# Performance work log

Measured on AMD Instinct MI355X. Metric: run time of the kernel, lower is better.

The kernel has to match this reference:

```python
import jax, jax.numpy as jnp
import numpy as np

HEADS = 8
DIM_HEAD = 64
SCALE = DIM_HEAD ** -0.5
K = 7


def _conv(x, w, stride):
    return jax.lax.conv_general_dilated(
        x, w, window_strides=(stride, stride), padding='VALID',
        dimension_numbers=('NHWC', 'HWIO', 'NHWC'))


def _split_heads(t):
    # 'b x y (h d) -> (b h) (x y) d'
    b, X, Y, hd = t.shape
    d = hd // HEADS
    t = t.reshape(b, X, Y, HEADS, d)
    t = t.transpose(0, 3, 1, 2, 4)  # b h x y d
    return t.reshape(b * HEADS, X * Y, d)


def setup_inputs() -> dict:
    key = jax.random.key(0)
    ks = jax.random.split(key, 6)
    dim, inner = 256, HEADS * DIM_HEAD
    x = jax.random.normal(ks[0], (8, 84, 84, dim), dtype=jnp.float32)
    w_q = jax.random.normal(ks[1], (1, 1, dim, inner), dtype=jnp.float32) * 0.02
    w_kv = jax.random.normal(ks[2], (K, K, dim, 2 * inner), dtype=jnp.float32) * 0.02
    w_out = jax.random.normal(ks[3], (1, 1, inner, dim), dtype=jnp.float32) * 0.02
    b_out = jnp.zeros((dim,), dtype=jnp.float32)
    return {"x": x, "w_q": w_q, "w_kv": w_kv, "w_out": w_out, "b_out": b_out}


def reference(x, w_q, w_kv, w_out, b_out):
    b, X, Y, _ = x.shape
    q = _conv(x, w_q, 1)          # [b, X, Y, inner]
    kv = _conv(x, w_kv, K)        # [b, X/k, Y/k, 2*inner]
    k, v = jnp.split(kv, 2, axis=-1)
    q = _split_heads(q)           # [(b h), XY, d]
    k = _split_heads(k)           # [(b h), xy, d]
    v = _split_heads(v)
    dots = jnp.einsum('bid,bjd->bij', q, k) * SCALE
    attn = jax.nn.softmax(dots, axis=-1)
    out = jnp.einsum('bij,bjd->bid', attn, v)  # [(b h), XY, d]
    out = out.reshape(b, HEADS, X, Y, DIM_HEAD).transpose(0, 2, 3, 1, 4)
    out = out.reshape(b, X, Y, HEADS * DIM_HEAD)
    out = _conv(out, w_out, 1) + b_out  # dropout rate 0 -> identity
    return out
```

## Files before the change

### kernel.cpp

```cpp
#include <hip/hip_runtime.h>

typedef unsigned short u16;
typedef __bf16 bf16x8 __attribute__((ext_vector_type(8)));
typedef __bf16 bf16x4 __attribute__((ext_vector_type(4)));
typedef float f32x4 __attribute__((ext_vector_type(4)));

__device__ __forceinline__ u16 f2b(float f) {
    __bf16 h = (__bf16)f;
    return __builtin_bit_cast(u16, h);
}
__device__ __forceinline__ unsigned pk2(float a, float b) {
    return (unsigned)f2b(a) | ((unsigned)f2b(b) << 16);
}

__device__ __forceinline__ int xcd_chunk(int wg, int n) {
    int q = n >> 3, r = n & 7;
    int x = wg & 7, i = wg >> 3;
    return (x < r ? x * (q + 1) : r * (q + 1) + (x - r) * q) + i;
}

#define GLOAD_LDS16(src, dst)                                              \
    __builtin_amdgcn_global_load_lds(                                      \
        (const __attribute__((address_space(1))) void*)(src),              \
        (__attribute__((address_space(3))) void*)(dst), 16, 0, 0)

__global__ __launch_bounds__(256) void k_pack_x(const float* __restrict__ x,
                                                u16* __restrict__ xp) {
    int v = blockIdx.x * 256 + threadIdx.x;
    int c0 = (v & 31) << 3;
    int pix = v >> 5;
    int b = pix / 7056;
    int r = pix - b * 7056;
    int y = r / 84;
    int xx = r - y * 84;
    int opix = (b * 144 + (y / 7) * 12 + (xx / 7)) * 49 + (y % 7) * 7 + (xx % 7);
    const float4* src = reinterpret_cast<const float4*>(x + ((size_t)pix << 8) + c0);
    float4 f0 = src[0], f1 = src[1];
    bf16x8 o = {(__bf16)f0.x, (__bf16)f0.y, (__bf16)f0.z, (__bf16)f0.w,
                (__bf16)f1.x, (__bf16)f1.y, (__bf16)f1.z, (__bf16)f1.w};
    *reinterpret_cast<bf16x8*>(xp + ((size_t)opix << 8) + c0) = o;
}

__global__ __launch_bounds__(256) void k_lut(int* __restrict__ lut) {
    int q = blockIdx.x * 256 + threadIdx.x;
    if (q >= 7056) return;
    int pi = q / 49, pos = q - pi * 49;
    int y = (pi / 12) * 7 + pos / 7;
    int xx = (pi - (pi / 12) * 12) * 7 + (pos - (pos / 7) * 7);
    lut[q] = y * 84 + xx;
}

__global__ __launch_bounds__(256) void k_tconv(const float* __restrict__ in,
                                               u16* __restrict__ out, int R, int C,
                                               float scale, int permk) {
    __shared__ float tile[32][33];
    int c0 = blockIdx.x << 5, r0 = blockIdx.y << 5;
    int tx = threadIdx.x, ty = threadIdx.y;
#pragma unroll
    for (int i = 0; i < 4; i++)
        tile[ty + (i << 3)][tx] = in[(size_t)(r0 + ty + (i << 3)) * C + c0 + tx];
    __syncthreads();
    int k = r0 + tx;
    int kw = permk ? ((k & ~63) | ((k & 15) << 2) | ((k >> 4) & 3)) : k;
#pragma unroll
    for (int i = 0; i < 4; i++)
        out[(size_t)(c0 + ty + (i << 3)) * R + kw] = f2b(tile[tx][ty + (i << 3)] * scale);
}

__global__ __launch_bounds__(256) void k_kvproj(const u16* __restrict__ xp,
                                                const u16* __restrict__ wkvT,
                                                float* __restrict__ parts) {
    __shared__ u16 As[8192];
    __shared__ u16 Bs[8192];
    const int lin = xcd_chunk(blockIdx.x, 504);
    const int mt = lin % 9;
    const int rest = lin / 9;
    const int nt = rest & 7;
    const int sp = rest >> 3;
    const int tid = threadIdx.x;
    const int wave = tid >> 6, lane = tid & 63;
    const int wr = wave >> 1, wc = wave & 1;
    const int lrow = lane & 15, lkg = lane >> 4;
    const u16* Ag = xp + (size_t)(mt * 128) * 12544 + sp * 1792;
    const u16* Bg = wkvT + (size_t)(nt * 128) * 12544 + sp * 1792;
    const int srow = lane >> 3;
    const int scol_sw = (((lane & 7) ^ srow) << 3);
    f32x4 acc[4][4];
#pragma unroll
    for (int m = 0; m < 4; m++)
#pragma unroll
        for (int n = 0; n < 4; n++)
#pragma unroll
            for (int i = 0; i < 4; i++) acc[m][n][i] = 0.f;

    for (int ks = 0; ks < 28; ks++) {
        const int k0 = ks << 6;
        __syncthreads();
#pragma unroll
        for (int j = 0; j < 4; j++) {
            const int c = (wave << 2) + j;
            const int row = (c << 3) + srow;
            GLOAD_LDS16(Ag + (size_t)row * 12544 + k0 + scol_sw, As + (c << 9));
            GLOAD_LDS16(Bg + (size_t)row * 12544 + k0 + scol_sw, Bs + (c << 9));
        }
        __syncthreads();
#pragma unroll
        for (int kk = 0; kk < 2; kk++) {
            const int sig = (kk << 2) + lkg;
            const int sw = ((sig ^ (lrow & 7)) << 3);
            bf16x8 a[4], bb[4];
#pragma unroll
            for (int m = 0; m < 4; m++)
                a[m] = *reinterpret_cast<const bf16x8*>(As + (((wr << 6) + (m << 4) + lrow) << 6) + sw);
#pragma unroll
            for (int n = 0; n < 4; n++)
                bb[n] = *reinterpret_cast<const bf16x8*>(Bs + (((wc << 6) + (n << 4) + lrow) << 6) + sw);
#pragma unroll
            for (int m = 0; m < 4; m++)
#pragma unroll
                for (int n = 0; n < 4; n++)
                    acc[m][n] = __builtin_amdgcn_mfma_f32_16x16x32_bf16(a[m], bb[n], acc[m][n], 0, 0, 0);
        }
    }
    float* outp = parts + (size_t)sp * 1179648;
#pragma unroll
    for (int m = 0; m < 4; m++)
#pragma unroll
        for (int n = 0; n < 4; n++)
#pragma unroll
            for (int i = 0; i < 4; i++) {
                int row = (mt << 7) + (wr << 6) + (m << 4) + (lkg << 2) + i;
                int col = (nt << 7) + (wc << 6) + (n << 4) + lrow;
                outp[(size_t)row * 1024 + col] = acc[m][n][i];
            }
}

__global__ __launch_bounds__(256) void k_kvfin(const float* __restrict__ parts,
                                               u16* __restrict__ Kf, u16* __restrict__ Vf) {
    int v = blockIdx.x * 256 + threadIdx.x;
    int m = v >> 8;
    int n0 = (v & 255) << 2;
    float4 s = {0.f, 0.f, 0.f, 0.f};
#pragma unroll
    for (int sp = 0; sp < 7; sp++) {
        float4 p = *reinterpret_cast<const float4*>(parts + (size_t)sp * 1179648 +
                                                    (size_t)m * 1024 + n0);
        s.x += p.x; s.y += p.y; s.z += p.z; s.w += p.w;
    }
    int b = m / 144, pi = m - b * 144;
    float sv[4] = {s.x, s.y, s.z, s.w};
#pragma unroll
    for (int e4 = 0; e4 < 4; e4++) {
        int n = n0 + e4;
        int h = (n & 511) >> 6, d = n & 63;
        int bh = (b << 3) + h;
        if (n < 512) {
            int fc = pi >> 4, lr = pi & 15;
            int ks = d >> 5, lg = (d >> 3) & 3, e = d & 7;
            Kf[((((size_t)bh * 9 + fc) << 1) + ks) * 512 + (((lg << 4) + lr) << 3) + e] = f2b(sv[e4]);
        } else {
            int nf = d >> 4, lr = d & 15;
            int ks = pi >> 5;
            int e = (((pi >> 4) & 1) << 2) | (pi & 3);
            int lg = (pi >> 2) & 3;
            Vf[(((size_t)bh * 4 + nf) * 5 + ks) * 512 + (((lg << 4) + lr) << 3) + e] = f2b(sv[e4]);
        }
    }
}

__global__ __launch_bounds__(256) void k_qproj(const u16* __restrict__ xp,
                                               const u16* __restrict__ wqT,
                                               u16* __restrict__ Qf) {
    __shared__ u16 As[8192];
    __shared__ u16 Bs[8192];
    const int lin = xcd_chunk(blockIdx.x, 1764);
    const int nt = lin & 3, mt = lin >> 2;
    const int tid = threadIdx.x;
    const int wave = tid >> 6, lane = tid & 63;
    const int wr = wave >> 1, wc = wave & 1;
    const int lrow = lane & 15, lkg = lane >> 4;
    const u16* Ag = xp + (size_t)(mt * 128) * 256;
    const u16* Bg = wqT + (size_t)(nt * 128) * 256;
    const int srow = lane >> 3;
    const int scol_sw = (((lane & 7) ^ srow) << 3);
    f32x4 acc[4][4];
#pragma unroll
    for (int m = 0; m < 4; m++)
#pragma unroll
        for (int n = 0; n < 4; n++)
#pragma unroll
            for (int i = 0; i < 4; i++) acc[m][n][i] = 0.f;

    for (int ks = 0; ks < 4; ks++) {
        const int k0 = ks << 6;
        __syncthreads();
#pragma unroll
        for (int j = 0; j < 4; j++) {
            const int c = (wave << 2) + j;
            const int row = (c << 3) + srow;
            GLOAD_LDS16(Ag + (size_t)row * 256 + k0 + scol_sw, As + (c << 9));
            GLOAD_LDS16(Bg + (size_t)row * 256 + k0 + scol_sw, Bs + (c << 9));
        }
        __syncthreads();
#pragma unroll
        for (int kk = 0; kk < 2; kk++) {
            const int sig = (kk << 2) + lkg;
            const int sw = ((sig ^ (lrow & 7)) << 3);
            bf16x8 a[4], bb[4];
#pragma unroll
            for (int m = 0; m < 4; m++)
                a[m] = *reinterpret_cast<const bf16x8*>(As + (((wr << 6) + (m << 4) + lrow) << 6) + sw);
#pragma unroll
            for (int n = 0; n < 4; n++)
                bb[n] = *reinterpret_cast<const bf16x8*>(Bs + (((wc << 6) + (n << 4) + lrow) << 6) + sw);
#pragma unroll
            for (int m = 0; m < 4; m++)
#pragma unroll
                for (int n = 0; n < 4; n++)
                    acc[m][n] = __builtin_amdgcn_mfma_f32_16x16x32_bf16(a[m], bb[n], acc[m][n], 0, 0, 0);
        }
    }
#pragma unroll
    for (int m = 0; m < 4; m++)
#pragma unroll
        for (int n = 0; n < 4; n++)
#pragma unroll
            for (int i = 0; i < 4; i++) {
                int row = (mt << 7) + (wr << 6) + (m << 4) + (lkg << 2) + i;
                int col = (nt << 7) + (wc << 6) + (n << 4) + lrow;
                int b = row / 7056, pp = row - b * 7056;
                int h = col >> 6, d = col & 63;
                int bh = (b << 3) + h;
                int tt = pp >> 4, flr = pp & 15;
                int fks = d >> 5, flg = (d >> 3) & 3, fe = d & 7;
                Qf[((((size_t)bh * 441 + tt) << 1) + fks) * 512 + (((flg << 4) + flr) << 3) + fe] =
                    f2b(acc[m][n][i]);
            }
}

__global__ __launch_bounds__(128, 2) void k_attn(const u16* __restrict__ Qf,
                                                 const u16* __restrict__ Kf,
                                                 const u16* __restrict__ Vf,
                                                 const int* __restrict__ lut,
                                                 u16* __restrict__ O) {
    const int wv = threadIdx.x >> 6, lane = threadIdx.x & 63;
    const int h = (blockIdx.y << 1) + wv;
    const int b = blockIdx.z;
    const int lrow = lane & 15, lkg = lane >> 4;
    const int bh = (b << 3) + h;
    const int l8 = lane << 3;

    const u16* Kg = Kf + (((size_t)bh * 9) << 10);
    const u16* Vg = Vf + ((size_t)bh * 20) * 512;

    bf16x8 kf[9][2], vf[4][5];
#pragma unroll
    for (int fc = 0; fc < 9; fc++)
#pragma unroll
        for (int ks = 0; ks < 2; ks++)
            kf[fc][ks] = *reinterpret_cast<const bf16x8*>(Kg + (((fc << 1) + ks) << 9) + l8);
#pragma unroll
    for (int n = 0; n < 4; n++)
#pragma unroll
        for (int ks = 0; ks < 5; ks++)
            vf[n][ks] = *reinterpret_cast<const bf16x8*>(Vg + ((size_t)(n * 5 + ks) << 9) + l8);

    const int t0 = blockIdx.x * 3;
#pragma unroll 1
    for (int jt = 0; jt < 3; jt++) {
        const int t = t0 + jt;
        const u16* Qg = Qf + ((((size_t)bh * 441 + t) << 1) << 9);

        f32x4 da[9];
#pragma unroll
        for (int fc = 0; fc < 9; fc++)
#pragma unroll
            for (int i = 0; i < 4; i++) da[fc][i] = 0.f;
#pragma unroll
        for (int ks = 0; ks < 2; ks++) {
            bf16x8 aq = *reinterpret_cast<const bf16x8*>(Qg + (ks << 9) + l8);
#pragma unroll
            for (int fc = 0; fc < 9; fc++)
                da[fc] = __builtin_amdgcn_mfma_f32_16x16x32_bf16(kf[fc][ks], aq, da[fc], 0, 0, 0);
        }

        float mx = -1e30f;
#pragma unroll
        for (int fc = 0; fc < 9; fc++)
#pragma unroll
            for (int i = 0; i < 4; i++) mx = fmaxf(mx, da[fc][i]);
        mx = fmaxf(mx, __shfl_xor(mx, 16));
        mx = fmaxf(mx, __shfl_xor(mx, 32));
        float sum = 0.f;
#pragma unroll
        for (int fc = 0; fc < 9; fc++)
#pragma unroll
            for (int i = 0; i < 4; i++) {
                float v = __expf(da[fc][i] - mx);
                da[fc][i] = v;
                sum += v;
            }
        sum += __shfl_xor(sum, 16);
        sum += __shfl_xor(sum, 32);
        float inv = 1.0f / sum;
        unsigned pw[9][2];
#pragma unroll
        for (int fc = 0; fc < 9; fc++) {
            pw[fc][0] = pk2(da[fc][0] * inv, da[fc][1] * inv);
            pw[fc][1] = pk2(da[fc][2] * inv, da[fc][3] * inv);
        }

        f32x4 oa[4];
#pragma unroll
        for (int n = 0; n < 4; n++)
#pragma unroll
            for (int i = 0; i < 4; i++) oa[n][i] = 0.f;
#pragma unroll
        for (int ks = 0; ks < 5; ks++) {
            uint4 pav;
            if (ks < 4)
                pav = uint4{pw[2 * ks][0], pw[2 * ks][1], pw[2 * ks + 1][0], pw[2 * ks + 1][1]};
            else
                pav = uint4{pw[8][0], pw[8][1], 0u, 0u};
            bf16x8 pa = __builtin_bit_cast(bf16x8, pav);
#pragma unroll
            for (int n = 0; n < 4; n++)
                oa[n] = __builtin_amdgcn_mfma_f32_16x16x32_bf16(pa, vf[n][ks], oa[n], 0, 0, 0);
        }

#pragma unroll
        for (int i = 0; i < 4; i++) {
            int q = (t << 4) + (lkg << 2) + i;
            int rast = lut[q];
            bf16x4 ov = {(__bf16)oa[0][i], (__bf16)oa[1][i], (__bf16)oa[2][i], (__bf16)oa[3][i]};
            *reinterpret_cast<bf16x4*>(O + (((size_t)b * 7056 + rast) << 9) +
                                       (h << 6) + (lrow << 2)) = ov;
        }
    }
}

__global__ __launch_bounds__(256) void k_outproj(const u16* __restrict__ A,
                                                 const u16* __restrict__ BT,
                                                 const float* __restrict__ bias,
                                                 float* __restrict__ out) {
    __shared__ u16 As[128][72];
    __shared__ u16 Bs[128][72];
    const int lin = xcd_chunk(blockIdx.x, 882);
    const int nt = lin & 1, mt = lin >> 1;
    const int tid = threadIdx.x;
    const int wave = tid >> 6, lane = tid & 63;
    const int wr = wave >> 1, wc = wave & 1;
    const int lrow = lane & 15, lkg = lane >> 4;
    const u16* Ag = A + (size_t)(mt * 128) * 512;
    const u16* Bg = BT + (size_t)(nt * 128) * 512;
    const int srow = tid >> 3, scol = (tid & 7) << 3;
    f32x4 acc[4][4];
#pragma unroll
    for (int m = 0; m < 4; m++)
#pragma unroll
        for (int n = 0; n < 4; n++)
#pragma unroll
            for (int i = 0; i < 4; i++) acc[m][n][i] = 0.f;

    for (int ks = 0; ks < 8; ks++) {
        const int k0 = ks * 64;
        __syncthreads();
#pragma unroll
        for (int p = 0; p < 4; p++) {
            int rr = srow + (p << 5);
            *reinterpret_cast<bf16x8*>(&As[rr][scol]) =
                *reinterpret_cast<const bf16x8*>(Ag + (size_t)rr * 512 + k0 + scol);
            *reinterpret_cast<bf16x8*>(&Bs[rr][scol]) =
                *reinterpret_cast<const bf16x8*>(Bg + (size_t)rr * 512 + k0 + scol);
        }
        __syncthreads();
#pragma unroll
        for (int kk = 0; kk < 2; kk++) {
            const int ko = (kk << 5) + (lkg << 3);
            bf16x8 a[4], bb[4];
#pragma unroll
            for (int m = 0; m < 4; m++)
                a[m] = *reinterpret_cast<const bf16x8*>(&As[(wr << 6) + (m << 4) + lrow][ko]);
#pragma unroll
            for (int n = 0; n < 4; n++)
                bb[n] = *reinterpret_cast<const bf16x8*>(&Bs[(wc << 6) + (n << 4) + lrow][ko]);
#pragma unroll
            for (int m = 0; m < 4; m++)
#pragma unroll
                for (int n = 0; n < 4; n++)
                    acc[m][n] = __builtin_amdgcn_mfma_f32_16x16x32_bf16(a[m], bb[n], acc[m][n], 0, 0, 0);
        }
    }
#pragma unroll
    for (int m = 0; m < 4; m++)
#pragma unroll
        for (int n = 0; n < 4; n++)
#pragma unroll
            for (int i = 0; i < 4; i++) {
                int row = (mt << 7) + (wr << 6) + (m << 4) + (lkg << 2) + i;
                int col = (nt << 7) + (wc << 6) + (n << 4) + lrow;
                out[(size_t)row * 256 + col] = acc[m][n][i] + bias[col];
            }
}

extern "C" void kernel_launch(void* const* d_in, const int* in_sizes, int n_in,
                              void* d_out, int out_size, void* d_ws, size_t ws_size,
                              hipStream_t stream) {
    const float* x = (const float*)d_in[0];
    const float* w_q = (const float*)d_in[1];
    const float* w_kv = (const float*)d_in[2];
    const float* w_out = (const float*)d_in[3];
    const float* b_out = (const float*)d_in[4];
    float* out = (float*)d_out;

    char* ws = (char*)d_ws;
    size_t off = 0;
    auto alloc = [&](size_t bytes) -> char* {
        char* p = ws + off;
        off = (off + bytes + 255) & ~(size_t)255;
        return p;
    };
    u16* xp = (u16*)alloc(28901376ull);
    u16* wqT = (u16*)alloc(262144ull);
    u16* woutT = (u16*)alloc(262144ull);
    u16* Kf = (u16*)alloc(1179648ull);
    u16* Vf = (u16*)alloc(1310720ull);
    int* lut = (int*)alloc(28416ull);
    u16* O = (u16*)alloc(57802752ull);
    u16* wkvT = (u16*)alloc(25690112ull);
    float* parts = (float*)alloc(33030144ull);
    u16* Qf = (u16*)wkvT;

    hipMemsetAsync(Vf, 0, 1310720ull, stream);
    k_lut<<<28, 256, 0, stream>>>(lut);
    k_pack_x<<<7056, 256, 0, stream>>>(x, xp);
    k_tconv<<<dim3(32, 392), dim3(32, 8), 0, stream>>>(w_kv, wkvT, 12544, 1024, 1.0f, 0);
    k_tconv<<<dim3(16, 8), dim3(32, 8), 0, stream>>>(w_q, wqT, 256, 512, 0.125f, 0);
    k_tconv<<<dim3(8, 16), dim3(32, 8), 0, stream>>>(w_out, woutT, 512, 256, 1.0f, 1);
    k_kvproj<<<504, 256, 0, stream>>>(xp, wkvT, parts);
    k_kvfin<<<1152, 256, 0, stream>>>(parts, Kf, Vf);
    k_qproj<<<1764, 256, 0, stream>>>(xp, wqT, Qf);
    k_attn<<<dim3(147, 4, 8), 128, 0, stream>>>(Qf, Kf, Vf, lut, O);
    k_outproj<<<882, 256, 0, stream>>>(O, woutT, b_out, out);
}
```

Baseline: 205.0 us.

## Fuse output projection into attention kernel via shared-memory staging

Each attention block now runs all 8 heads for one batch and tile, writes the per-head outputs into shared memory, then multiplies them by a pre-fragmented w_out with MFMA and writes the final fp32 result plus bias directly. This removes the separate out-projection GEMM and the round trip of the large bf16 O intermediate through global memory. In exchange each block does extra synchronisation and reads w_out fragments from global or L2 on every tile. The block also grows to 512 threads, which may lower occupancy.

```diff
diff --git a/kernel.cpp b/kernel.cpp
--- a/kernel.cpp
+++ b/kernel.cpp
@@ -52,7 +52,7 @@
 
 __global__ __launch_bounds__(256) void k_tconv(const float* __restrict__ in,
                                                u16* __restrict__ out, int R, int C,
-                                               float scale, int permk) {
+                                               float scale) {
     __shared__ float tile[32][33];
     int c0 = blockIdx.x << 5, r0 = blockIdx.y << 5;
     int tx = threadIdx.x, ty = threadIdx.y;
@@ -61,10 +61,19 @@
         tile[ty + (i << 3)][tx] = in[(size_t)(r0 + ty + (i << 3)) * C + c0 + tx];
     __syncthreads();
     int k = r0 + tx;
-    int kw = permk ? ((k & ~63) | ((k & 15) << 2) | ((k >> 4) & 3)) : k;
 #pragma unroll
     for (int i = 0; i < 4; i++)
-        out[(size_t)(c0 + ty + (i << 3)) * R + kw] = f2b(tile[tx][ty + (i << 3)] * scale);
+        out[(size_t)(c0 + ty + (i << 3)) * R + k] = f2b(tile[tx][ty + (i << 3)] * scale);
+}
+
+__global__ __launch_bounds__(256) void k_wofrag(const float* __restrict__ w_out,
+                                               u16* __restrict__ woFrag) {
+    int v = blockIdx.x * 256 + threadIdx.x;
+    int k = v >> 8, outcol = v & 255;
+    int kw = (k & ~63) | ((k & 15) << 2) | ((k >> 4) & 3);
+    int nf = outcol >> 4, lr = outcol & 15;
+    int ks = kw >> 5, lg = (kw >> 3) & 3, e = kw & 7;
+    woFrag[((((nf << 4) + ks) << 6) + (lg << 4) + lr) * 8 + e] = f2b(w_out[v]);
 }
 
 __global__ __launch_bounds__(256) void k_kvproj(const u16* __restrict__ xp,
@@ -238,14 +247,17 @@
             }
 }
 
-__global__ __launch_bounds__(128, 2) void k_attn(const u16* __restrict__ Qf,
-                                                 const u16* __restrict__ Kf,
-                                                 const u16* __restrict__ Vf,
-                                                 const int* __restrict__ lut,
-                                                 u16* __restrict__ O) {
+__global__ __launch_bounds__(512, 2) void k_attn_out(const u16* __restrict__ Qf,
+                                                     const u16* __restrict__ Kf,
+                                                     const u16* __restrict__ Vf,
+                                                     const int* __restrict__ lut,
+                                                     const u16* __restrict__ woFrag,
+                                                     const float* __restrict__ bias,
+                                                     float* __restrict__ out) {
+    __shared__ u16 Osm[16 * 520];
     const int wv = threadIdx.x >> 6, lane = threadIdx.x & 63;
-    const int h = (blockIdx.y << 1) + wv;
-    const int b = blockIdx.z;
+    const int h = wv;
+    const int b = blockIdx.y;
     const int lrow = lane & 15, lkg = lane >> 4;
     const int bh = (b << 3) + h;
     const int l8 = lane << 3;
@@ -264,6 +276,10 @@
 #pragma unroll
         for (int ks = 0; ks < 5; ks++)
             vf[n][ks] = *reinterpret_cast<const bf16x8*>(Vg + ((size_t)(n * 5 + ks) << 9) + l8);
+
+    const int nf0 = wv << 1;
+    const float bias0 = bias[(nf0 << 4) + lrow];
+    const float bias1 = bias[((nf0 + 1) << 4) + lrow];
 
     const int t0 = blockIdx.x * 3;
 #pragma unroll 1
@@ -330,77 +346,32 @@
 
 #pragma unroll
         for (int i = 0; i < 4; i++) {
+            int q = (lkg << 2) + i;
+            bf16x4 ov = {(__bf16)oa[0][i], (__bf16)oa[1][i], (__bf16)oa[2][i], (__bf16)oa[3][i]};
+            *reinterpret_cast<bf16x4*>(&Osm[q * 520 + (h << 6) + (lrow << 2)]) = ov;
+        }
+        __syncthreads();
+
+        f32x4 oc0, oc1;
+#pragma unroll
+        for (int i = 0; i < 4; i++) { oc0[i] = 0.f; oc1[i] = 0.f; }
+#pragma unroll
+        for (int ks = 0; ks < 16; ks++) {
+            bf16x8 a = *reinterpret_cast<const bf16x8*>(&Osm[lrow * 520 + (ks << 5) + (lkg << 3)]);
+            bf16x8 b0 = *reinterpret_cast<const bf16x8*>(woFrag + ((((nf0 << 4) + ks) << 6) << 3) + l8);
+            bf16x8 b1 = *reinterpret_cast<const bf16x8*>(woFrag + (((((nf0 + 1) << 4) + ks) << 6) << 3) + l8);
+            oc0 = __builtin_amdgcn_mfma_f32_16x16x32_bf16(a, b0, oc0, 0, 0, 0);
+            oc1 = __builtin_amdgcn_mfma_f32_16x16x32_bf16(a, b1, oc1, 0, 0, 0);
+        }
+#pragma unroll
+        for (int i = 0; i < 4; i++) {
             int q = (t << 4) + (lkg << 2) + i;
-            int rast = lut[q];
-            bf16x4 ov = {(__bf16)oa[0][i], (__bf16)oa[1][i], (__bf16)oa[2][i], (__bf16)oa[3][i]};
-            *reinterpret_cast<bf16x4*>(O + (((size_t)b * 7056 + rast) << 9) +
-                                       (h << 6) + (lrow << 2)) = ov;
-        }
+            float* op = out + ((size_t)b * 7056 + lut[q]) * 256;
+            op[(nf0 << 4) + lrow] = oc0[i] + bias0;
+            op[((nf0 + 1) << 4) + lrow] = oc1[i] + bias1;
+        }
+        __syncthreads();
     }
-}
-
-__global__ __launch_bounds__(256) void k_outproj(const u16* __restrict__ A,
-                                                 const u16* __restrict__ BT,
-                                                 const float* __restrict__ bias,
-                                                 float* __restrict__ out) {
-    __shared__ u16 As[128][72];
-    __shared__ u16 Bs[128][72];
-    const int lin = xcd_chunk(blockIdx.x, 882);
-    const int nt = lin & 1, mt = lin >> 1;
-    const int tid = threadIdx.x;
-    const int wave = tid >> 6, lane = tid & 63;
-    const int wr = wave >> 1, wc = wave & 1;
-    const int lrow = lane & 15, lkg = lane >> 4;
-    const u16* Ag = A + (size_t)(mt * 128) * 512;
-    const u16* Bg = BT + (size_t)(nt * 128) * 512;
-    const int srow = tid >> 3, scol = (tid & 7) << 3;
-    f32x4 acc[4][4];
-#pragma unroll
-    for (int m = 0; m < 4; m++)
-#pragma unroll
-        for (int n = 0; n < 4; n++)
-#pragma unroll
-            for (int i = 0; i < 4; i++) acc[m][n][i] = 0.f;
-
-    for (int ks = 0; ks < 8; ks++) {
-        const int k0 = ks * 64;
-        __syncthreads();
-#pragma unroll
-        for (int p = 0; p < 4; p++) {
-            int rr = srow + (p << 5);
-            *reinterpret_cast<bf16x8*>(&As[rr][scol]) =
-                *reinterpret_cast<const bf16x8*>(Ag + (size_t)rr * 512 + k0 + scol);
-            *reinterpret_cast<bf16x8*>(&Bs[rr][scol]) =
-                *reinterpret_cast<const bf16x8*>(Bg + (size_t)rr * 512 + k0 + scol);
-        }
-        __syncthreads();
-#pragma unroll
-        for (int kk = 0; kk < 2; kk++) {
-            const int ko = (kk << 5) + (lkg << 3);
-            bf16x8 a[4], bb[4];
-#pragma unroll
-            for (int m = 0; m < 4; m++)
-                a[m] = *reinterpret_cast<const bf16x8*>(&As[(wr << 6) + (m << 4) + lrow][ko]);
-#pragma unroll
-            for (int n = 0; n < 4; n++)
-                bb[n] = *reinterpret_cast<const bf16x8*>(&Bs[(wc << 6) + (n << 4) + lrow][ko]);
-#pragma unroll
-            for (int m = 0; m < 4; m++)
-#pragma unroll
-                for (int n = 0; n < 4; n++)
-                    acc[m][n] = __builtin_amdgcn_mfma_f32_16x16x32_bf16(a[m], bb[n], acc[m][n], 0, 0, 0);
-        }
-    }
-#pragma unroll
-    for (int m = 0; m < 4; m++)
-#pragma unroll
-        for (int n = 0; n < 4; n++)
-#pragma unroll
-            for (int i = 0; i < 4; i++) {
-                int row = (mt << 7) + (wr << 6) + (m << 4) + (lkg << 2) + i;
-                int col = (nt << 7) + (wc << 6) + (n << 4) + lrow;
-                out[(size_t)row * 256 + col] = acc[m][n][i] + bias[col];
-            }
 }
 
 extern "C" void kernel_launch(void* const* d_in, const int* in_sizes, int n_in,
@@ -422,11 +393,10 @@
     };
     u16* xp = (u16*)alloc(28901376ull);
     u16* wqT = (u16*)alloc(262144ull);
-    u16* woutT = (u16*)alloc(262144ull);
+    u16* woFrag = (u16*)alloc(262144ull);
     u16* Kf = (u16*)alloc(1179648ull);
     u16* Vf = (u16*)alloc(1310720ull);
     int* lut = (int*)alloc(28416ull);
-    u16* O = (u16*)alloc(57802752ull);
     u16* wkvT = (u16*)alloc(25690112ull);
     float* parts = (float*)alloc(33030144ull);
     u16* Qf = (u16*)wkvT;
@@ -434,12 +404,11 @@
     hipMemsetAsync(Vf, 0, 1310720ull, stream);
     k_lut<<<28, 256, 0, stream>>>(lut);
     k_pack_x<<<7056, 256, 0, stream>>>(x, xp);
-    k_tconv<<<dim3(32, 392), dim3(32, 8), 0, stream>>>(w_kv, wkvT, 12544, 1024, 1.0f, 0);
-    k_tconv<<<dim3(16, 8), dim3(32, 8), 0, stream>>>(w_q, wqT, 256, 512, 0.125f, 0);
-    k_tconv<<<dim3(8, 16), dim3(32, 8), 0, stream>>>(w_out, woutT, 512, 256, 1.0f, 1);
+    k_tconv<<<dim3(32, 392), dim3(32, 8), 0, stream>>>(w_kv, wkvT, 12544, 1024, 1.0f);
+    k_tconv<<<dim3(16, 8), dim3(32, 8), 0, stream>>>(w_q, wqT, 256, 512, 0.125f);
+    k_wofrag<<<512, 256, 0, stream>>>(w_out, woFrag);
     k_kvproj<<<504, 256, 0, stream>>>(xp, wkvT, parts);
     k_kvfin<<<1152, 256, 0, stream>>>(parts, Kf, Vf);
     k_qproj<<<1764, 256, 0, stream>>>(xp, wqT, Qf);
-    k_attn<<<dim3(147, 4, 8), 128, 0, stream>>>(Qf, Kf, Vf, lut, O);
-    k_outproj<<<882, 256, 0, stream>>>(O, woutT, b_out, out);
-}
+    k_attn_out<<<dim3(147, 8), 512, 0, stream>>>(Qf, Kf, Vf, lut, woFrag, b_out, out);
+}
```

New measurement: 343.2 us. 67.4% more time.
